# Kernel optimization log

Hardware: AMD Instinct MI355X
Metric: run time of the kernel (lower is better)

The kernel has to match this reference:

```python
import jax, jax.numpy as jnp
import numpy as np
import math

B, S, F, D = 8, 2048, 1024, 1024
NEG = -1e9


def setup_inputs() -> dict:
    key = jax.random.key(0)
    ks = jax.random.split(key, 5)
    x = jax.random.normal(ks[0], (B, S, F), dtype=jnp.float32)
    r_mat = jax.random.normal(ks[1], (B, S, S), dtype=jnp.float32)
    # shared causal attention mask [S, S] (1 = keep, 0 = masked)
    attn_mask = jnp.tril(jnp.ones((S, S), dtype=jnp.float32))
    # per-batch padding mask [B, 1, S]: last 128 tokens of half the batch padded
    pad = jnp.ones((B, 1, S), dtype=jnp.float32)
    pad = pad.at[B // 2:, :, S - 128:].set(0.0)
    Wq = jax.random.normal(ks[2], (F, D), dtype=jnp.float32) / math.sqrt(F)
    Wk = jax.random.normal(ks[3], (F, D), dtype=jnp.float32) / math.sqrt(F)
    Wv = jax.random.normal(ks[4], (F, D), dtype=jnp.float32) / math.sqrt(F)
    return {"x": x, "r_mat": r_mat, "attn_mask": attn_mask, "pad_mask": pad,
            "Wq": Wq, "Wk": Wk, "Wv": Wv}


def reference(x, r_mat, attn_mask, pad_mask, Wq, Wk, Wv):
    scale = math.sqrt(x.shape[-1])  # original scales by sqrt(features)
    q = jnp.einsum('bsf,fd->bsd', x, Wq)
    k = jnp.einsum('bsf,fd->bsd', x, Wk)
    v = jnp.einsum('bsf,fd->bsd', x, Wv)
    scores = jnp.einsum('bsd,btd->bst', q, k) / scale  # [B, S, S]
    keep = (pad_mask != 0.0) & (attn_mask[None] != 0.0)  # [B, S, S] broadcast
    r = jnp.where(keep, r_mat, NEG)
    r = jax.nn.softmax(r, axis=-1)
    scores = jnp.where(keep, scores + r, NEG)
    prob = jax.nn.softmax(scores, axis=-1)
    return jnp.einsum('bst,btd->bsd', prob, v)
```

## Files before the change

kernel.cpp:

```cpp
#include <hip/hip_runtime.h>
#include <hip/hip_bf16.h>

#define B_ 8
#define S_ 2048
#define F_ 1024
#define D_ 1024

typedef unsigned short u16;
typedef float f32x4 __attribute__((ext_vector_type(4)));
typedef __bf16 bf16x8 __attribute__((ext_vector_type(8)));
typedef unsigned short u16x8 __attribute__((ext_vector_type(8)));

__device__ __forceinline__ u16 f2bf(float f) {
  union { float f; unsigned u; } v; v.f = f;
  unsigned r = v.u + 0x7fff + ((v.u >> 16) & 1);
  return (u16)(r >> 16);
}
__device__ __forceinline__ float bf2f(u16 b) {
  union { unsigned u; float f; } v; v.u = ((unsigned)b) << 16;
  return v.f;
}

__device__ __forceinline__ void stage16(const u16* g, u16* l) {
  __builtin_amdgcn_global_load_lds(
      (const __attribute__((address_space(1))) void*)g,
      (__attribute__((address_space(3))) void*)l, 16, 0, 0);
}

__device__ __forceinline__ int xcd_swz(int f, int n) {
  int per = n >> 3;
  return (f & 7) * per + (f >> 3);
}


__global__ void cast_x(const float* __restrict__ x, u16* __restrict__ xb, int n4) {
  int i = blockIdx.x * blockDim.x + threadIdx.x;
  int stride = gridDim.x * blockDim.x;
  for (; i < n4; i += stride) {
    float4 v = ((const float4*)x)[i];
    ushort4 o;
    o.x = f2bf(v.x); o.y = f2bf(v.y); o.z = f2bf(v.z); o.w = f2bf(v.w);
    ((ushort4*)xb)[i] = o;
  }
}

__global__ void transW(const float* __restrict__ Wq, const float* __restrict__ Wk,
                       const float* __restrict__ Wv, u16* __restrict__ Wt) {
  __shared__ float tile[32][33];
  int z = blockIdx.z;
  const float* W = (z == 0) ? Wq : ((z == 1) ? Wk : Wv);
  int f0 = blockIdx.y * 32, d0 = blockIdx.x * 32;
  int tx = threadIdx.x & 31, ty = threadIdx.x >> 5;
  for (int i = 0; i < 4; i++)
    tile[ty + i * 8][tx] = W[(size_t)(f0 + ty + i * 8) * D_ + d0 + tx];
  __syncthreads();
  u16* o = Wt + (size_t)z * D_ * F_;
  for (int i = 0; i < 4; i++)
    o[(size_t)(d0 + ty + i * 8) * F_ + f0 + tx] = f2bf(tile[tx][ty + i * 8]);
}

__global__ __launch_bounds__(256) void r_rowsum(const float* __restrict__ r,
                                                const float* __restrict__ pm,
                                                float* __restrict__ rs) {
  int row = blockIdx.x;
  int b = row >> 11, s = row & 2047;
  const float4* rp = (const float4*)(r + (size_t)row * S_);
  const float4* pp = (const float4*)(pm + (size_t)b * S_);
  int nv = (s >> 2) + 1;
  float acc = 0.f;
  for (int i = threadIdx.x; i < nv; i += 256) {
    float4 rv = rp[i];
    float4 pv = pp[i];
    int t0 = i << 2;
    #pragma unroll
    for (int j = 0; j < 4; j++) {
      int t = t0 + j;
      if (t <= s && (&pv.x)[j] != 0.f) acc += __expf((&rv.x)[j] - 16.f);
    }
  }
  for (int off = 1; off < 64; off <<= 1) acc += __shfl_xor(acc, off);
  __shared__ float wsum[4];
  int lane = threadIdx.x & 63, w = threadIdx.x >> 6;
  if (lane == 0) wsum[w] = acc;
  __syncthreads();
  if (threadIdx.x == 0) rs[row] = wsum[0] + wsum[1] + wsum[2] + wsum[3];
}


__device__ __forceinline__ bf16x8 readfrag(const u16* lds, int row, int ks, int hi) {
  int c = ((ks << 6) + (hi << 4)) ^ ((row & 7) << 4);
  return *(const bf16x8*)((const char*)lds + row * 128 + c);
}

#define SYNC_POINT()                                                             \
  __builtin_amdgcn_sched_barrier(0);                                             \
  __builtin_amdgcn_s_barrier();                                                  \
  __builtin_amdgcn_sched_barrier(0);


__device__ __forceinline__ void stageA(const u16* __restrict__ src, int ld, int h,
                                       u16* ldsA, int w, int l) {
  int base = ((w >> 2) * 128) + h * 64 + ((w & 3) * 16);
  int r = l >> 3, ch = (l & 7) ^ (l >> 3);
  #pragma unroll
  for (int i = 0; i < 2; i++) {
    int row = base + i * 8;
    stage16(src + (size_t)(row + r) * ld + ch * 8, ldsA + row * 64);
  }
}
__device__ __forceinline__ void stageB(const u16* __restrict__ src, int ld, int h,
                                       u16* ldsB, int w, int l) {
  int base = h * 128 + w * 16;
  int r = l >> 3, ch = (l & 7) ^ (l >> 3);
  #pragma unroll
  for (int i = 0; i < 2; i++) {
    int row = base + i * 8;
    stage16(src + (size_t)(row + r) * ld + ch * 8, ldsB + row * 64);
  }
}

#define MFMAQ(AF, KB, MB)                                                        \
  __builtin_amdgcn_s_setprio(1);                                                 \
  _Pragma("unroll")                                                              \
  for (int m = 0; m < 4; m++)                                                    \
    _Pragma("unroll")                                                            \
    for (int n = 0; n < 4; n++)                                                  \
      acc[(MB) + m][n] = __builtin_amdgcn_mfma_f32_16x16x32_bf16(                \
          AF[m], bfr[(KB) + n], acc[(MB) + m][n], 0, 0, 0);                      \
  __builtin_amdgcn_s_setprio(0);

__device__ __forceinline__ void gemm256(const u16* __restrict__ A, int lda,
                                        const u16* __restrict__ B, int ldb,
                                        int nT, u16* lds, f32x4 acc[8][4]) {
  const int t = threadIdx.x, w = t >> 6, l = t & 63;
  const int wr = w >> 2, wc = w & 3;
  u16* A0 = lds;           u16* B0 = lds + 16384;
  u16* A1 = lds + 32768;   u16* B1 = lds + 49152;

  #pragma unroll
  for (int m = 0; m < 8; m++)
    #pragma unroll
    for (int n = 0; n < 4; n++)
      #pragma unroll
      for (int j = 0; j < 4; j++) acc[m][n][j] = 0.f;

  stageB(B, ldb, 0, B0, w, l);
  stageB(B, ldb, 1, B0, w, l);
  stageA(A, lda, 0, A0, w, l);
  stageA(A, lda, 1, A0, w, l);
  if (nT > 1) stageA(A + 64, lda, 0, A1, w, l);
  asm volatile("s_waitcnt vmcnt(4)" ::: "memory");
  SYNC_POINT()

  const int arow = wr * 128 + (l & 15), brow = wc * 64 + (l & 15), hi = l >> 4;

  for (int kt = 0; kt < nT; kt++) {
    u16* cA = (kt & 1) ? A1 : A0;
    u16* cB = (kt & 1) ? B1 : B0;
    u16* nA = (kt & 1) ? A0 : A1;
    u16* nB = (kt & 1) ? B0 : B1;
    const u16* An1 = A + (size_t)(kt + 1) * 64;
    const u16* Bn1 = B + (size_t)(kt + 1) * 64;
    const u16* An2 = A + (size_t)(kt + 2) * 64;
    const bool has1 = (kt + 1 < nT), has2 = (kt + 2 < nT);
    bf16x8 af0[4], af1[4], bfr[8];

    #pragma unroll
    for (int m = 0; m < 4; m++) af0[m] = readfrag(cA, arow + m * 16, 0, hi);
    #pragma unroll
    for (int n = 0; n < 4; n++) bfr[n] = readfrag(cB, brow + n * 16, 0, hi);
    #pragma unroll
    for (int m = 0; m < 4; m++) af1[m] = readfrag(cA, arow + m * 16, 1, hi);
    #pragma unroll
    for (int n = 0; n < 4; n++) bfr[4 + n] = readfrag(cB, brow + n * 16, 1, hi);
    if (has1) stageB(Bn1, ldb, 0, nB, w, l);
    MFMAQ(af0, 0, 0)

    if (has1) {
      stageB(Bn1, ldb, 1, nB, w, l);
      asm volatile("s_waitcnt vmcnt(4)" ::: "memory");
    } else {
      asm volatile("s_waitcnt vmcnt(0)" ::: "memory");
    }
    SYNC_POINT()
    MFMAQ(af1, 4, 0)

    #pragma unroll
    for (int m = 0; m < 4; m++) af0[m] = readfrag(cA, arow + 64 + m * 16, 0, hi);
    #pragma unroll
    for (int m = 0; m < 4; m++) af1[m] = readfrag(cA, arow + 64 + m * 16, 1, hi);
    if (has2) stageA(An2, lda, 0, cA, w, l);
    MFMAQ(af0, 0, 4)

    if (has1) stageA(An1, lda, 1, nA, w, l);
    if (has1 && has2)  { asm volatile("s_waitcnt vmcnt(4)" ::: "memory"); }
    else if (has1)     { asm volatile("s_waitcnt vmcnt(2)" ::: "memory"); }
    else               { asm volatile("s_waitcnt vmcnt(0)" ::: "memory"); }
    SYNC_POINT()
    MFMAQ(af1, 4, 4)
  }
}

__device__ __forceinline__ void store256_bf16(f32x4 acc[8][4], u16* smem,
                                              u16* dst, int ld) {
  int t = threadIdx.x, w = t >> 6, l = t & 63;
  int wr = w >> 2, wc = w & 3;
  #pragma unroll
  for (int q = 0; q < 4; q++) {
    __syncthreads();
    if (wr == (q >> 1)) {
      int mb = (q & 1) * 4;
      #pragma unroll
      for (int mm = 0; mm < 4; mm++)
        #pragma unroll
        for (int j = 0; j < 4; j++) {
          int row = mm * 16 + (l >> 4) * 4 + j;
          #pragma unroll
          for (int n = 0; n < 4; n++)
            smem[row * 264 + wc * 64 + n * 16 + (l & 15)] = f2bf(acc[mb + mm][n][j]);
        }
    }
    __syncthreads();
    #pragma unroll
    for (int i = 0; i < 4; i++) {
      int idx = i * 512 + t;
      int row = idx >> 5, ch = idx & 31;
      *(u16x8*)(dst + (size_t)(q * 64 + row) * ld + ch * 8) =
          *(const u16x8*)(smem + row * 264 + ch * 8);
    }
  }
}

__global__ __launch_bounds__(512, 2) void gemm_qkv(
    const u16* __restrict__ xb, const u16* __restrict__ Wt,
    u16* __restrict__ qb, u16* __restrict__ kb, u16* __restrict__ vT) {
  __shared__ __align__(16) u16 lds[65536];
  int f = xcd_swz(blockIdx.x + 64 * blockIdx.y + 256 * blockIdx.z, 768);
  int bx = f & 63, by = (f >> 6) & 3, z = f >> 8;
  f32x4 acc[8][4];
  if (z < 2) {
    int m0 = bx * 256, n0 = by * 256;
    gemm256(xb + (size_t)m0 * F_, F_,
            Wt + (size_t)z * D_ * F_ + (size_t)n0 * F_, F_, F_ / 64, lds, acc);
    store256_bf16(acc, lds, ((z == 0) ? qb : kb) + (size_t)m0 * D_ + n0, D_);
  } else {
    int d0 = by * 256, s0g = bx * 256;
    gemm256(Wt + 2ULL * D_ * F_ + (size_t)d0 * F_, F_,
            xb + (size_t)s0g * F_, F_, F_ / 64, lds, acc);
    int b = s0g >> 11, s0 = s0g & 2047;
    store256_bf16(acc, lds, vT + (size_t)b * D_ * S_ + (size_t)d0 * S_ + s0, S_);
  }
}


__device__ __forceinline__ void stage128(const u16* __restrict__ src, int ld, int h,
                                         u16* ldsT, int w, int l) {
  int base = h * 64 + w * 16;
  int r = l >> 3, ch = (l & 7) ^ (l >> 3);
  #pragma unroll
  for (int i = 0; i < 2; i++) {
    int row = base + i * 8;
    stage16(src + (size_t)(row + r) * ld + ch * 8, ldsT + row * 64);
  }
}

#define MFMA16(AF, BF)                                                           \
  __builtin_amdgcn_s_setprio(1);                                                 \
  _Pragma("unroll")                                                              \
  for (int m = 0; m < 4; m++)                                                    \
    _Pragma("unroll")                                                            \
    for (int n = 0; n < 4; n++)                                                  \
      acc[m][n] = __builtin_amdgcn_mfma_f32_16x16x32_bf16(                       \
          AF[m], BF[n], acc[m][n], 0, 0, 0);                                     \
  __builtin_amdgcn_s_setprio(0);

__device__ __forceinline__ void gemm128(const u16* __restrict__ A, int lda,
                                        const u16* __restrict__ B, int ldb,
                                        int nT, u16* lds, f32x4 acc[4][4]) {
  const int t = threadIdx.x, w = t >> 6, l = t & 63;
  const int wr = w >> 1, wc = w & 1;
  u16* A0 = lds;          u16* B0 = lds + 8192;
  u16* A1 = lds + 16384;  u16* B1 = lds + 24576;

  #pragma unroll
  for (int m = 0; m < 4; m++)
    #pragma unroll
    for (int n = 0; n < 4; n++)
      #pragma unroll
      for (int j = 0; j < 4; j++) acc[m][n][j] = 0.f;

  stage128(A, lda, 0, A0, w, l);
  stage128(A, lda, 1, A0, w, l);
  stage128(B, ldb, 0, B0, w, l);
  stage128(B, ldb, 1, B0, w, l);
  if (nT > 1) {
    stage128(A + 64, lda, 0, A1, w, l);
    stage128(A + 64, lda, 1, A1, w, l);
    asm volatile("s_waitcnt vmcnt(4)" ::: "memory");
  } else {
    asm volatile("s_waitcnt vmcnt(0)" ::: "memory");
  }
  SYNC_POINT()

  const int arow = wr * 64 + (l & 15), brow = wc * 64 + (l & 15), hi = l >> 4;

  for (int kt = 0; kt < nT; kt++) {
    u16* cA = (kt & 1) ? A1 : A0;
    u16* cB = (kt & 1) ? B1 : B0;
    u16* nB = (kt & 1) ? B0 : B1;
    const bool has1 = (kt + 1 < nT), has2 = (kt + 2 < nT);
    bf16x8 a0f[4], b0f[4], a1f[4], b1f[4];

    #pragma unroll
    for (int m = 0; m < 4; m++) a0f[m] = readfrag(cA, arow + m * 16, 0, hi);
    #pragma unroll
    for (int n = 0; n < 4; n++) b0f[n] = readfrag(cB, brow + n * 16, 0, hi);
    #pragma unroll
    for (int m = 0; m < 4; m++) a1f[m] = readfrag(cA, arow + m * 16, 1, hi);
    #pragma unroll
    for (int n = 0; n < 4; n++) b1f[n] = readfrag(cB, brow + n * 16, 1, hi);
    if (has1) {
      stage128(B + (size_t)(kt + 1) * 64, ldb, 0, nB, w, l);
      stage128(B + (size_t)(kt + 1) * 64, ldb, 1, nB, w, l);
    }
    MFMA16(a0f, b0f)
    asm volatile("s_waitcnt lgkmcnt(0)" ::: "memory");
    SYNC_POINT()

    if (has2) {
      stage128(A + (size_t)(kt + 2) * 64, lda, 0, cA, w, l);
      stage128(A + (size_t)(kt + 2) * 64, lda, 1, cA, w, l);
    }
    MFMA16(a1f, b1f)
    if (has2)      { asm volatile("s_waitcnt vmcnt(4)" ::: "memory"); }
    else if (has1) { asm volatile("s_waitcnt vmcnt(0)" ::: "memory"); }
    SYNC_POINT()
  }
}

__global__ __launch_bounds__(256, 2) void attn_scores(
    const u16* __restrict__ qb, const u16* __restrict__ kb,
    const float* __restrict__ r_mat, const float* __restrict__ pm,
    const float* __restrict__ rs_r, u16* __restrict__ P,
    float* __restrict__ rowsum) {
  __shared__ __align__(16) u16 lds[32768];
  int f = xcd_swz(blockIdx.x + 136 * blockIdx.y, 1088);
  int x = f % 136, b = f / 136;
  int mt = (int)((sqrtf(8.f * x + 1.f) - 1.f) * 0.5f);
  while ((mt + 1) * (mt + 2) / 2 <= x) mt++;
  while (mt * (mt + 1) / 2 > x) mt--;
  int nt = x - mt * (mt + 1) / 2;
  int m0 = mt * 128, n0 = nt * 128;
  f32x4 acc[4][4];
  gemm128(qb + ((size_t)b * S_ + m0) * D_, D_,
          kb + ((size_t)b * S_ + n0) * D_, D_, D_ / 64, lds, acc);
  int t = threadIdx.x, w = t >> 6, l = t & 63;
  int wr = w >> 1, wc = w & 1;
  float* fs = (float*)lds;
  const float* rb = r_mat + (size_t)b * S_ * S_;
  const float* pmp = pm + (size_t)b * S_ + n0;
  #pragma unroll
  for (int h = 0; h < 2; h++) {
    __syncthreads();
    if (wr == h) {
      #pragma unroll
      for (int m = 0; m < 4; m++)
        #pragma unroll
        for (int j = 0; j < 4; j++) {
          int row = m * 16 + (l >> 4) * 4 + j;
          #pragma unroll
          for (int n = 0; n < 4; n++)
            fs[row * 132 + wc * 64 + n * 16 + (l & 15)] = acc[m][n][j];
        }
    }
    __syncthreads();
    int row = t >> 2, cg = t & 3;
    int srow = m0 + h * 64 + row;
    float invr = 1.f / rs_r[b * S_ + srow];
    const float* rrow = rb + (size_t)srow * S_ + n0 + cg * 32;
    u16* prow = P + (size_t)b * S_ * S_ + (size_t)srow * S_ + n0 + cg * 32;
    const float* fsc = fs + row * 132 + cg * 32;
    float rsum = 0.f;
    #pragma unroll
    for (int cc = 0; cc < 4; cc++) {
      int ch = (cg + cc) & 3;
      f32x4 q0 = *(const f32x4*)(fsc + ch * 8);
      f32x4 q1 = *(const f32x4*)(fsc + ch * 8 + 4);
      f32x4 r0 = *(const f32x4*)(rrow + ch * 8);
      f32x4 r1 = *(const f32x4*)(rrow + ch * 8 + 4);
      f32x4 p0 = *(const f32x4*)(pmp + cg * 32 + ch * 8);
      f32x4 p1 = *(const f32x4*)(pmp + cg * 32 + ch * 8 + 4);
      u16x8 o;
      #pragma unroll
      for (int k = 0; k < 8; k++) {
        int tc = n0 + cg * 32 + ch * 8 + k;
        float rv = (k < 4) ? r0[k] : r1[k - 4];
        float pmv = (k < 4) ? p0[k] : p1[k - 4];
        float qk = (k < 4) ? q0[k] : q1[k - 4];
        bool keep = (tc <= srow) && (pmv != 0.f);
        float rsm = __expf(rv - 16.f) * invr;
        float e = keep ? __expf(fmaf(qk, 0.03125f, rsm - 16.f)) : 0.f;
        u16 pb = f2bf(e); o[k] = pb; rsum += bf2f(pb);
      }
      *(u16x8*)(prow + ch * 8) = o;
    }
    rsum += __shfl_xor(rsum, 1);
    rsum += __shfl_xor(rsum, 2);
    if ((t & 3) == 0) atomicAdd(&rowsum[b * S_ + srow], rsum);
  }
}

__global__ __launch_bounds__(256, 2) void attn_pv(
    const u16* __restrict__ P, const u16* __restrict__ vT,
    const float* __restrict__ rowsum, float* __restrict__ out) {
  __shared__ __align__(16) u16 lds[32768];
  int f = xcd_swz(blockIdx.x + 16 * blockIdx.y + 128 * blockIdx.z, 1024);
  int mt = 15 - (f & 15), dt = (f >> 4) & 7, b = f >> 7;
  int m0 = mt * 128, n0 = dt * 128;
  int nT = (m0 + 128) / 64;
  f32x4 acc[4][4];
  gemm128(P + ((size_t)b * S_ + m0) * S_, S_,
          vT + ((size_t)b * D_ + n0) * S_, S_, nT, lds, acc);
  int t = threadIdx.x, w = t >> 6, l = t & 63;
  int wr = w >> 1, wc = w & 1;
  float* fs = (float*)lds;
  #pragma unroll
  for (int h = 0; h < 2; h++) {
    __syncthreads();
    if (wr == h) {
      #pragma unroll
      for (int m = 0; m < 4; m++)
        #pragma unroll
        for (int j = 0; j < 4; j++) {
          int row = m * 16 + (l >> 4) * 4 + j;
          float inv = 1.f / rowsum[b * S_ + m0 + h * 64 + row];
          #pragma unroll
          for (int n = 0; n < 4; n++)
            fs[row * 132 + wc * 64 + n * 16 + (l & 15)] = acc[m][n][j] * inv;
        }
    }
    __syncthreads();
    #pragma unroll
    for (int i = 0; i < 8; i++) {
      int idx = i * 256 + t;
      int row = idx >> 5, c4 = (idx & 31) << 2;
      *(float4*)(out + ((size_t)b * S_ + m0 + h * 64 + row) * D_ + n0 + c4) =
          *(const float4*)(fs + row * 132 + c4);
    }
  }
}

extern "C" void kernel_launch(void* const* d_in, const int* in_sizes, int n_in,
                              void* d_out, int out_size, void* d_ws, size_t ws_size,
                              hipStream_t stream) {
  const float* x     = (const float*)d_in[0];
  const float* r_mat = (const float*)d_in[1];
  const float* pm    = (const float*)d_in[3];
  const float* Wq    = (const float*)d_in[4];
  const float* Wk    = (const float*)d_in[5];
  const float* Wv    = (const float*)d_in[6];
  float* out = (float*)d_out;
  char* ws = (char*)d_ws;

  u16*   qb     = (u16*)(ws + 0);
  u16*   kb     = (u16*)(ws + 33554432ULL);
  u16*   vT     = (u16*)(ws + 67108864ULL);
  float* rs_r   = (float*)(ws + 100663296ULL);
  float* rowsum = (float*)(ws + 100728832ULL);
  u16*   P      = (u16*)(ws + 100794368ULL);
  u16*   xb     = (u16*)(ws + 100794368ULL);
  u16*   Wt     = (u16*)(ws + 134348800ULL);

  cast_x<<<dim3(2048), dim3(256), 0, stream>>>(x, xb, (B_ * S_ * F_) / 4);
  transW<<<dim3(32, 32, 3), dim3(256), 0, stream>>>(Wq, Wk, Wv, Wt);
  r_rowsum<<<dim3(B_ * S_), dim3(256), 0, stream>>>(r_mat, pm, rs_r);
  gemm_qkv<<<dim3(64, 4, 3), dim3(512), 0, stream>>>(xb, Wt, qb, kb, vT);
  hipMemsetAsync(rowsum, 0, B_ * S_ * sizeof(float), stream);
  attn_scores<<<dim3(136, 8), dim3(256), 0, stream>>>(qb, kb, r_mat, pm, rs_r, P, rowsum);
  attn_pv<<<dim3(16, 8, 8), dim3(256), 0, stream>>>(P, vT, rowsum, out);
}
```

Measured before the change: 280.8 us.

## Pack P into triangular tiles and precompute bf16 r-softmax term per tile

Adds an er_pass kernel that computes the masked r-softmax once and writes it as bf16 in a packed lower-triangular tile layout, with -1e9 for masked entries. The scores kernel then reads that bf16 tile instead of fp32 r_mat and the pad mask, and writes P in the same packed layout that attn_pv reads with a fixed 128 stride. This cuts scores-stage traffic and strided access. The cost is an extra pass over r_mat, extra workspace, and bf16 rounding of the r term. It also removes the XCD swizzle in gemm_qkv and keeps a fallback path when the workspace is too small.

New measurement: 274.0 us. 1.02x faster.

```diff
diff --git a/kernel.cpp b/kernel.cpp
--- a/kernel.cpp
+++ b/kernel.cpp
@@ -5,6 +5,8 @@
 #define S_ 2048
 #define F_ 1024
 #define D_ 1024
+#define TRI_ 136
+#define TELEM_ 16384
 
 typedef unsigned short u16;
 typedef float f32x4 __attribute__((ext_vector_type(4)));
@@ -59,6 +61,62 @@
     o[(size_t)(d0 + ty + i * 8) * F_ + f0 + tx] = f2bf(tile[tx][ty + i * 8]);
 }
 
+__global__ __launch_bounds__(256) void er_pass(const float* __restrict__ r,
+                                               const float* __restrict__ pm,
+                                               u16* __restrict__ er,
+                                               float* __restrict__ rs_r) {
+  int row = blockIdx.x;
+  int b = row >> 11, s = row & 2047;
+  const float4* rp = (const float4*)(r + (size_t)row * S_);
+  const float4* pp = (const float4*)(pm + (size_t)b * S_);
+  int nk = (s >> 2) + 1;
+  int nw = ((s >> 7) + 1) << 5;
+  float4 ev[8];
+  float acc = 0.f;
+  #pragma unroll
+  for (int it = 0; it < 8; it++) {
+    int i = threadIdx.x + it * 256;
+    if (i < nk) {
+      float4 rv = rp[i], pv = pp[i];
+      int t0 = i << 2;
+      float4 e;
+      #pragma unroll
+      for (int j = 0; j < 4; j++) {
+        bool keep = (t0 + j <= s) && ((&pv.x)[j] != 0.f);
+        (&e.x)[j] = keep ? __expf((&rv.x)[j] - 16.f) : 0.f;
+        acc += (&e.x)[j];
+      }
+      ev[it] = e;
+    }
+  }
+  for (int off = 1; off < 64; off <<= 1) acc += __shfl_xor(acc, off);
+  __shared__ float wsum[4];
+  int lane = threadIdx.x & 63, w = threadIdx.x >> 6;
+  if (lane == 0) wsum[w] = acc;
+  __syncthreads();
+  float total = wsum[0] + wsum[1] + wsum[2] + wsum[3];
+  if (threadIdx.x == 0) rs_r[row] = total;
+  float invr = 1.f / total;
+  int c = s >> 7, rin = s & 127;
+  u16* tb = er + (size_t)(b * TRI_ + c * (c + 1) / 2) * TELEM_ + rin * 128;
+  #pragma unroll
+  for (int it = 0; it < 8; it++) {
+    int i = threadIdx.x + it * 256;
+    if (i < nw) {
+      int t0 = i << 2;
+      float4 pv = pp[i];
+      ushort4 o;
+      #pragma unroll
+      for (int j = 0; j < 4; j++) {
+        bool keep = (t0 + j <= s) && ((&pv.x)[j] != 0.f);
+        float val = keep ? (&ev[it].x)[j] * invr : -1e9f;
+        (&o.x)[j] = f2bf(val);
+      }
+      *(ushort4*)(tb + (size_t)(t0 >> 7) * TELEM_ + (t0 & 127)) = o;
+    }
+  }
+}
+
 __global__ __launch_bounds__(256) void r_rowsum(const float* __restrict__ r,
                                                 const float* __restrict__ pm,
                                                 float* __restrict__ rs) {
@@ -235,16 +293,15 @@
     const u16* __restrict__ xb, const u16* __restrict__ Wt,
     u16* __restrict__ qb, u16* __restrict__ kb, u16* __restrict__ vT) {
   __shared__ __align__(16) u16 lds[65536];
-  int f = xcd_swz(blockIdx.x + 64 * blockIdx.y + 256 * blockIdx.z, 768);
-  int bx = f & 63, by = (f >> 6) & 3, z = f >> 8;
+  int z = blockIdx.z;
   f32x4 acc[8][4];
   if (z < 2) {
-    int m0 = bx * 256, n0 = by * 256;
+    int m0 = blockIdx.x * 256, n0 = blockIdx.y * 256;
     gemm256(xb + (size_t)m0 * F_, F_,
             Wt + (size_t)z * D_ * F_ + (size_t)n0 * F_, F_, F_ / 64, lds, acc);
     store256_bf16(acc, lds, ((z == 0) ? qb : kb) + (size_t)m0 * D_ + n0, D_);
   } else {
-    int d0 = by * 256, s0g = bx * 256;
+    int d0 = blockIdx.y * 256, s0g = blockIdx.x * 256;
     gemm256(Wt + 2ULL * D_ * F_ + (size_t)d0 * F_, F_,
             xb + (size_t)s0g * F_, F_, F_ / 64, lds, acc);
     int b = s0g >> 11, s0 = s0g & 2047;
@@ -253,27 +310,7 @@
 }
 
 
-__device__ __forceinline__ void stage128(const u16* __restrict__ src, int ld, int h,
-                                         u16* ldsT, int w, int l) {
-  int base = h * 64 + w * 16;
-  int r = l >> 3, ch = (l & 7) ^ (l >> 3);
-  #pragma unroll
-  for (int i = 0; i < 2; i++) {
-    int row = base + i * 8;
-    stage16(src + (size_t)(row + r) * ld + ch * 8, ldsT + row * 64);
-  }
-}
-
-#define MFMA16(AF, BF)                                                           \
-  __builtin_amdgcn_s_setprio(1);                                                 \
-  _Pragma("unroll")                                                              \
-  for (int m = 0; m < 4; m++)                                                    \
-    _Pragma("unroll")                                                            \
-    for (int n = 0; n < 4; n++)                                                  \
-      acc[m][n] = __builtin_amdgcn_mfma_f32_16x16x32_bf16(                       \
-          AF[m], BF[n], acc[m][n], 0, 0, 0);                                     \
-  __builtin_amdgcn_s_setprio(0);
-
+template <int PACKA>
 __device__ __forceinline__ void gemm128(const u16* __restrict__ A, int lda,
                                         const u16* __restrict__ B, int ldb,
                                         int nT, u16* lds, f32x4 acc[4][4]) {
@@ -282,6 +319,11 @@
   u16* A0 = lds;          u16* B0 = lds + 8192;
   u16* A1 = lds + 16384;  u16* B1 = lds + 24576;
 
+  auto asrc = [&](int kt) -> const u16* {
+    return PACKA ? A + (size_t)(kt >> 1) * TELEM_ + (kt & 1) * 64
+                 : A + (size_t)kt * 64;
+  };
+
   #pragma unroll
   for (int m = 0; m < 4; m++)
     #pragma unroll
@@ -289,13 +331,23 @@
       #pragma unroll
       for (int j = 0; j < 4; j++) acc[m][n][j] = 0.f;
 
-  stage128(A, lda, 0, A0, w, l);
-  stage128(A, lda, 1, A0, w, l);
-  stage128(B, ldb, 0, B0, w, l);
-  stage128(B, ldb, 1, B0, w, l);
+  auto stg = [&](const u16* src, int ld, int h, u16* dst) {
+    int base = h * 64 + w * 16;
+    int r = l >> 3, ch = (l & 7) ^ (l >> 3);
+    #pragma unroll
+    for (int i = 0; i < 2; i++) {
+      int row = base + i * 8;
+      stage16(src + (size_t)(row + r) * ld + ch * 8, dst + row * 64);
+    }
+  };
+
+  stg(asrc(0), PACKA ? 128 : lda, 0, A0);
+  stg(asrc(0), PACKA ? 128 : lda, 1, A0);
+  stg(B, ldb, 0, B0);
+  stg(B, ldb, 1, B0);
   if (nT > 1) {
-    stage128(A + 64, lda, 0, A1, w, l);
-    stage128(A + 64, lda, 1, A1, w, l);
+    stg(asrc(1), PACKA ? 128 : lda, 0, A1);
+    stg(asrc(1), PACKA ? 128 : lda, 1, A1);
     asm volatile("s_waitcnt vmcnt(4)" ::: "memory");
   } else {
     asm volatile("s_waitcnt vmcnt(0)" ::: "memory");
@@ -320,45 +372,59 @@
     #pragma unroll
     for (int n = 0; n < 4; n++) b1f[n] = readfrag(cB, brow + n * 16, 1, hi);
     if (has1) {
-      stage128(B + (size_t)(kt + 1) * 64, ldb, 0, nB, w, l);
-      stage128(B + (size_t)(kt + 1) * 64, ldb, 1, nB, w, l);
-    }
-    MFMA16(a0f, b0f)
+      stg(B + (size_t)(kt + 1) * 64, ldb, 0, nB);
+      stg(B + (size_t)(kt + 1) * 64, ldb, 1, nB);
+    }
+    __builtin_amdgcn_s_setprio(1);
+    #pragma unroll
+    for (int m = 0; m < 4; m++)
+      #pragma unroll
+      for (int n = 0; n < 4; n++)
+        acc[m][n] = __builtin_amdgcn_mfma_f32_16x16x32_bf16(a0f[m], b0f[n], acc[m][n], 0, 0, 0);
+    __builtin_amdgcn_s_setprio(0);
     asm volatile("s_waitcnt lgkmcnt(0)" ::: "memory");
     SYNC_POINT()
 
     if (has2) {
-      stage128(A + (size_t)(kt + 2) * 64, lda, 0, cA, w, l);
-      stage128(A + (size_t)(kt + 2) * 64, lda, 1, cA, w, l);
-    }
-    MFMA16(a1f, b1f)
+      stg(asrc(kt + 2), PACKA ? 128 : lda, 0, cA);
+      stg(asrc(kt + 2), PACKA ? 128 : lda, 1, cA);
+    }
+    __builtin_amdgcn_s_setprio(1);
+    #pragma unroll
+    for (int m = 0; m < 4; m++)
+      #pragma unroll
+      for (int n = 0; n < 4; n++)
+        acc[m][n] = __builtin_amdgcn_mfma_f32_16x16x32_bf16(a1f[m], b1f[n], acc[m][n], 0, 0, 0);
+    __builtin_amdgcn_s_setprio(0);
     if (has2)      { asm volatile("s_waitcnt vmcnt(4)" ::: "memory"); }
     else if (has1) { asm volatile("s_waitcnt vmcnt(0)" ::: "memory"); }
     SYNC_POINT()
   }
 }
 
-__global__ __launch_bounds__(256, 2) void attn_scores(
+__device__ __forceinline__ void tri_decode(int x, int& mt, int& nt) {
+  mt = (int)((sqrtf(8.f * x + 1.f) - 1.f) * 0.5f);
+  while ((mt + 1) * (mt + 2) / 2 <= x) mt++;
+  while (mt * (mt + 1) / 2 > x) mt--;
+  nt = x - mt * (mt + 1) / 2;
+}
+
+__global__ __launch_bounds__(256, 2) void attn_scores_er(
     const u16* __restrict__ qb, const u16* __restrict__ kb,
-    const float* __restrict__ r_mat, const float* __restrict__ pm,
-    const float* __restrict__ rs_r, u16* __restrict__ P,
+    const u16* __restrict__ er, u16* __restrict__ P,
     float* __restrict__ rowsum) {
   __shared__ __align__(16) u16 lds[32768];
   int f = xcd_swz(blockIdx.x + 136 * blockIdx.y, 1088);
   int x = f % 136, b = f / 136;
-  int mt = (int)((sqrtf(8.f * x + 1.f) - 1.f) * 0.5f);
-  while ((mt + 1) * (mt + 2) / 2 <= x) mt++;
-  while (mt * (mt + 1) / 2 > x) mt--;
-  int nt = x - mt * (mt + 1) / 2;
+  int mt, nt; tri_decode(x, mt, nt);
   int m0 = mt * 128, n0 = nt * 128;
   f32x4 acc[4][4];
-  gemm128(qb + ((size_t)b * S_ + m0) * D_, D_,
-          kb + ((size_t)b * S_ + n0) * D_, D_, D_ / 64, lds, acc);
+  gemm128<0>(qb + ((size_t)b * S_ + m0) * D_, D_,
+             kb + ((size_t)b * S_ + n0) * D_, D_, D_ / 64, lds, acc);
   int t = threadIdx.x, w = t >> 6, l = t & 63;
   int wr = w >> 1, wc = w & 1;
   float* fs = (float*)lds;
-  const float* rb = r_mat + (size_t)b * S_ * S_;
-  const float* pmp = pm + (size_t)b * S_ + n0;
+  size_t tbase = (size_t)(b * TRI_ + mt * (mt + 1) / 2 + nt) * TELEM_;
   #pragma unroll
   for (int h = 0; h < 2; h++) {
     __syncthreads();
@@ -375,10 +441,71 @@
     }
     __syncthreads();
     int row = t >> 2, cg = t & 3;
+    int rin = h * 64 + row;
+    const u16* et = er + tbase + (size_t)rin * 128 + cg * 32;
+    u16* pt = P + tbase + (size_t)rin * 128 + cg * 32;
+    const float* fsc = fs + row * 132 + cg * 32;
+    float rsum = 0.f;
+    #pragma unroll
+    for (int cc = 0; cc < 4; cc++) {
+      int ch = (cg + cc) & 3;
+      f32x4 q0 = *(const f32x4*)(fsc + ch * 8);
+      f32x4 q1 = *(const f32x4*)(fsc + ch * 8 + 4);
+      u16x8 e8 = *(const u16x8*)(et + ch * 8);
+      u16x8 o;
+      #pragma unroll
+      for (int k = 0; k < 8; k++) {
+        float qk = (k < 4) ? q0[k] : q1[k - 4];
+        float e = __expf(fmaf(qk, 0.03125f, bf2f(e8[k]) - 16.f));
+        u16 pb = f2bf(e); o[k] = pb; rsum += bf2f(pb);
+      }
+      *(u16x8*)(pt + ch * 8) = o;
+    }
+    rsum += __shfl_xor(rsum, 1);
+    rsum += __shfl_xor(rsum, 2);
+    if ((t & 3) == 0) atomicAdd(&rowsum[b * S_ + m0 + rin], rsum);
+  }
+}
+
+__global__ __launch_bounds__(256, 2) void attn_scores_rm(
+    const u16* __restrict__ qb, const u16* __restrict__ kb,
+    const float* __restrict__ r_mat, const float* __restrict__ pm,
+    const float* __restrict__ rs_r, u16* __restrict__ P,
+    float* __restrict__ rowsum) {
+  __shared__ __align__(16) u16 lds[32768];
+  int f = xcd_swz(blockIdx.x + 136 * blockIdx.y, 1088);
+  int x = f % 136, b = f / 136;
+  int mt, nt; tri_decode(x, mt, nt);
+  int m0 = mt * 128, n0 = nt * 128;
+  f32x4 acc[4][4];
+  gemm128<0>(qb + ((size_t)b * S_ + m0) * D_, D_,
+             kb + ((size_t)b * S_ + n0) * D_, D_, D_ / 64, lds, acc);
+  int t = threadIdx.x, w = t >> 6, l = t & 63;
+  int wr = w >> 1, wc = w & 1;
+  float* fs = (float*)lds;
+  const float* rb = r_mat + (size_t)b * S_ * S_;
+  const float* pmp = pm + (size_t)b * S_ + n0;
+  size_t tbase = (size_t)(b * TRI_ + mt * (mt + 1) / 2 + nt) * TELEM_;
+  #pragma unroll
+  for (int h = 0; h < 2; h++) {
+    __syncthreads();
+    if (wr == h) {
+      #pragma unroll
+      for (int m = 0; m < 4; m++)
+        #pragma unroll
+        for (int j = 0; j < 4; j++) {
+          int row = m * 16 + (l >> 4) * 4 + j;
+          #pragma unroll
+          for (int n = 0; n < 4; n++)
+            fs[row * 132 + wc * 64 + n * 16 + (l & 15)] = acc[m][n][j];
+        }
+    }
+    __syncthreads();
+    int row = t >> 2, cg = t & 3;
     int srow = m0 + h * 64 + row;
     float invr = 1.f / rs_r[b * S_ + srow];
     const float* rrow = rb + (size_t)srow * S_ + n0 + cg * 32;
-    u16* prow = P + (size_t)b * S_ * S_ + (size_t)srow * S_ + n0 + cg * 32;
+    u16* pt = P + tbase + (size_t)(h * 64 + row) * 128 + cg * 32;
     const float* fsc = fs + row * 132 + cg * 32;
     float rsum = 0.f;
     #pragma unroll
@@ -402,7 +529,7 @@
         float e = keep ? __expf(fmaf(qk, 0.03125f, rsm - 16.f)) : 0.f;
         u16 pb = f2bf(e); o[k] = pb; rsum += bf2f(pb);
       }
-      *(u16x8*)(prow + ch * 8) = o;
+      *(u16x8*)(pt + ch * 8) = o;
     }
     rsum += __shfl_xor(rsum, 1);
     rsum += __shfl_xor(rsum, 2);
@@ -417,10 +544,10 @@
   int f = xcd_swz(blockIdx.x + 16 * blockIdx.y + 128 * blockIdx.z, 1024);
   int mt = 15 - (f & 15), dt = (f >> 4) & 7, b = f >> 7;
   int m0 = mt * 128, n0 = dt * 128;
-  int nT = (m0 + 128) / 64;
+  int nT = 2 * (mt + 1);
   f32x4 acc[4][4];
-  gemm128(P + ((size_t)b * S_ + m0) * S_, S_,
-          vT + ((size_t)b * D_ + n0) * S_, S_, nT, lds, acc);
+  gemm128<1>(P + (size_t)(b * TRI_ + mt * (mt + 1) / 2) * TELEM_, 128,
+             vT + ((size_t)b * D_ + n0) * S_, S_, nT, lds, acc);
   int t = threadIdx.x, w = t >> 6, l = t & 63;
   int wr = w >> 1, wc = w & 1;
   float* fs = (float*)lds;
@@ -462,20 +589,30 @@
   float* out = (float*)d_out;
   char* ws = (char*)d_ws;
 
+  const size_t PK = (size_t)B_ * TRI_ * TELEM_ * 2;
   u16*   qb     = (u16*)(ws + 0);
   u16*   kb     = (u16*)(ws + 33554432ULL);
   u16*   vT     = (u16*)(ws + 67108864ULL);
-  float* rs_r   = (float*)(ws + 100663296ULL);
-  float* rowsum = (float*)(ws + 100728832ULL);
-  u16*   P      = (u16*)(ws + 100794368ULL);
+  float* rowsum = (float*)(ws + 100663296ULL);
+  float* rs_r   = (float*)(ws + 100728832ULL);
   u16*   xb     = (u16*)(ws + 100794368ULL);
   u16*   Wt     = (u16*)(ws + 134348800ULL);
+  u16*   er     = (u16*)(ws + 100794368ULL);
+  bool use_er   = ws_size >= 100794368ULL + 2 * PK;
+  u16*   P      = use_er ? (u16*)(ws + 100794368ULL + PK)
+                         : (u16*)(ws + 100794368ULL);
 
   cast_x<<<dim3(2048), dim3(256), 0, stream>>>(x, xb, (B_ * S_ * F_) / 4);
   transW<<<dim3(32, 32, 3), dim3(256), 0, stream>>>(Wq, Wk, Wv, Wt);
-  r_rowsum<<<dim3(B_ * S_), dim3(256), 0, stream>>>(r_mat, pm, rs_r);
+  if (!use_er)
+    r_rowsum<<<dim3(B_ * S_), dim3(256), 0, stream>>>(r_mat, pm, rs_r);
   gemm_qkv<<<dim3(64, 4, 3), dim3(512), 0, stream>>>(xb, Wt, qb, kb, vT);
   hipMemsetAsync(rowsum, 0, B_ * S_ * sizeof(float), stream);
-  attn_scores<<<dim3(136, 8), dim3(256), 0, stream>>>(qb, kb, r_mat, pm, rs_r, P, rowsum);
+  if (use_er) {
+    er_pass<<<dim3(B_ * S_), dim3(256), 0, stream>>>(r_mat, pm, er, rs_r);
+    attn_scores_er<<<dim3(136, 8), dim3(256), 0, stream>>>(qb, kb, er, P, rowsum);
+  } else {
+    attn_scores_rm<<<dim3(136, 8), dim3(256), 0, stream>>>(qb, kb, r_mat, pm, rs_r, P, rowsum);
+  }
   attn_pv<<<dim3(16, 8, 8), dim3(256), 0, stream>>>(P, vT, rowsum, out);
 }
```
